# Performance work log

Measured on AMD Instinct MI355X. Metric: run time of the kernel, lower is better.

The kernel has to match this reference:

```python
import jax, jax.numpy as jnp
import numpy as np

B, C, H, W = 8, 3, 1024, 1024
N_SPOTS = int(H * W * 0.015)  # 15728, matches torch: n = int(H*W*0.015)
KSIZE, SIGMA = 5, 1.5
RMAX = 3  # max snow-box radius (torch.randint(1, 4))


def setup_inputs() -> dict:
    key = jax.random.key(0)
    k1, k2, k3, k4 = jax.random.split(key, 4)
    x = jax.random.uniform(k1, (B, C, H, W), dtype=jnp.float32)
    ys = jax.random.randint(k2, (B, N_SPOTS), 0, H)
    xs = jax.random.randint(k3, (B, N_SPOTS), 0, W)
    rs = jax.random.randint(k4, (B, N_SPOTS), 0, 3)  # radius = rs + 1 in {1,2,3}
    return {"x": x, "ys": ys, "xs": xs, "rs": rs}


def _snow_mask(ys, xs, rs, h, w):
    # Union of axis-aligned boxes: pixel (py,px) is snow iff some spot has
    # |py - y| <= r and |px - x| <= r (box clipping to the image is equivalent).
    b, n = ys.shape
    r = rs + 1  # radii 1..3
    d = jnp.arange(-RMAX, RMAX + 1)
    dy = jnp.repeat(d, 2 * RMAX + 1)  # [49]
    dx = jnp.tile(d, 2 * RMAX + 1)    # [49]
    yy = ys[:, :, None] + dy  # [B, n, 49]
    xx = xs[:, :, None] + dx
    valid = ((jnp.abs(dy) <= r[:, :, None]) & (jnp.abs(dx) <= r[:, :, None])
             & (yy >= 0) & (yy < h) & (xx >= 0) & (xx < w))
    yy = jnp.where(valid, yy, h)  # out-of-bounds sentinel -> dropped by scatter
    xx = jnp.where(valid, xx, w)
    b_idx = jnp.broadcast_to(jnp.arange(b)[:, None, None], yy.shape)
    mask = jnp.zeros((b, h, w), dtype=bool)
    mask = mask.at[b_idx, yy, xx].set(True, mode="drop")
    return mask


def _gauss_kernel():
    coords = jnp.arange(KSIZE, dtype=jnp.float32) - KSIZE // 2
    g = jnp.exp(-coords ** 2 / (2.0 * SIGMA ** 2))
    g = g / g.sum()
    return jnp.outer(g, g)  # [5, 5]


def reference(x, ys, xs, rs):
    b, c, h, w = x.shape
    mask = _snow_mask(ys, xs, rs, h, w)                   # [B, H, W]
    out = jnp.where(mask[:, None, :, :], jnp.float32(0.95), x)
    kernel = jnp.broadcast_to(_gauss_kernel(), (c, 1, KSIZE, KSIZE))  # depthwise OIHW
    pad = KSIZE // 2
    out = jax.lax.conv_general_dilated(
        out, kernel, window_strides=(1, 1), padding=[(pad, pad), (pad, pad)],
        dimension_numbers=("NCHW", "OIHW", "NCHW"), feature_group_count=c)
    return jnp.clip(out, 0.0, 1.0)
```

## Files before the change

kernel.cpp:

```cpp
#include <hip/hip_runtime.h>

#define BB 8
#define CC 3
#define HH 1024
#define WW 1024
#define NS 15728

#define G0 0.1200784f
#define G1 0.2338808f
#define G2 0.2920816f

__global__ __launch_bounds__(256) void snow_mask_kernel(
    const int* __restrict__ ys, const int* __restrict__ xs,
    const int* __restrict__ rs, unsigned int* __restrict__ mbits) {
  int s = blockIdx.x * 256 + threadIdx.x;
  if (s >= NS) return;
  int b = blockIdx.y;
  int idx = b * NS + s;
  int y = ys[idx];
  int x = xs[idx];
  int r = rs[idx] + 1;
  int x0 = max(x - r, 0), x1 = min(x + r, WW - 1);
  int y0 = max(y - r, 0), y1 = min(y + r, HH - 1);
  int w0 = x0 >> 5, w1 = x1 >> 5;
  unsigned int m0 = 0xFFFFFFFFu << (x0 & 31);
  unsigned int m1 = 0xFFFFFFFFu >> (31 - (x1 & 31));
  for (int py = y0; py <= y1; ++py) {
    unsigned int* rowp = mbits + ((unsigned)(b * HH + py) << 5);
    if (w0 == w1) {
      atomicOr(&rowp[w0], m0 & m1);
    } else {
      atomicOr(&rowp[w0], m0);
      atomicOr(&rowp[w1], m1);
    }
  }
}

#define TS 140
#define NLOAD 2312

__global__ __launch_bounds__(256, 4) void snow_blur_kernel(
    const float* __restrict__ x, const unsigned int* __restrict__ mbits,
    float* __restrict__ out) {
  __shared__ float tile[68 * TS];

  const int bz = blockIdx.z;
  const int b = bz / CC;
  const int bx = blockIdx.x, by = blockIdx.y;
  const int tid = threadIdx.x;
  const float* __restrict__ xp = x + (size_t)bz * (HH * WW);
  const unsigned int* __restrict__ mb = mbits + ((unsigned)(b * HH) << 5);

  const int gxbase = bx * 128 - 4;
  const int gybase = by * 64 - 2;

  float4 v[10];
  unsigned int bits[10];
  int lidx[10];
#pragma unroll
  for (int k = 0; k < 10; ++k) {
    int i = tid + k * 256;
    i = i < (NLOAD - 1) ? i : (NLOAD - 1);
    int r = i / 34;
    int c4 = i - r * 34;
    int gy = gybase + r;
    int gx = gxbase + c4 * 4;
    int gyc = min(max(gy, 0), HH - 1);
    int gxc = min(max(gx, 0), WW - 4);
    v[k] = *(const float4*)(xp + (size_t)gyc * WW + gxc);
    unsigned int bm = (mb[(gyc << 5) + (gxc >> 5)] >> (gxc & 31)) & 0xFu;
    if ((gy != gyc) | (gx != gxc)) bm = 16u;
    bits[k] = bm;
    lidx[k] = r * TS + c4 * 4;
  }
#pragma unroll
  for (int k = 0; k < 10; ++k) {
    float4 t = v[k];
    unsigned int bm = bits[k];
    if (bm & 1u) t.x = 0.95f;
    if (bm & 2u) t.y = 0.95f;
    if (bm & 4u) t.z = 0.95f;
    if (bm & 8u) t.w = 0.95f;
    if (bm & 16u) { t.x = 0.f; t.y = 0.f; t.z = 0.f; t.w = 0.f; }
    *(float4*)&tile[lidx[k]] = t;
  }
  __syncthreads();

  const int c = tid & 31;
  const int ty = tid >> 5;
  const float* trow = tile + (ty * 8) * TS + c * 4;

  auto hrow = [&](int j, float4& h) {
    const float* p = trow + j * TS;
    float4 A = *(const float4*)(p);
    float4 Bv = *(const float4*)(p + 4);
    float2 Cv = *(const float2*)(p + 8);
    h.x = G0 * (A.z + Bv.z) + G1 * (A.w + Bv.y) + G2 * Bv.x;
    h.y = G0 * (A.w + Bv.w) + G1 * (Bv.x + Bv.z) + G2 * Bv.y;
    h.z = G0 * (Bv.x + Cv.x) + G1 * (Bv.y + Bv.w) + G2 * Bv.z;
    h.w = G0 * (Bv.y + Cv.y) + G1 * (Bv.z + Cv.x) + G2 * Bv.w;
  };

  float4 h0, h1, h2, h3, h4;
  hrow(0, h0); hrow(1, h1); hrow(2, h2); hrow(3, h3); hrow(4, h4);

  float* op = out + (size_t)bz * (HH * WW) +
              (size_t)(by * 64 + ty * 8) * WW + (bx * 128 + c * 4);
#pragma unroll
  for (int k = 0; k < 8; ++k) {
    float4 s;
    s.x = G0 * (h0.x + h4.x) + G1 * (h1.x + h3.x) + G2 * h2.x;
    s.y = G0 * (h0.y + h4.y) + G1 * (h1.y + h3.y) + G2 * h2.y;
    s.z = G0 * (h0.z + h4.z) + G1 * (h1.z + h3.z) + G2 * h2.z;
    s.w = G0 * (h0.w + h4.w) + G1 * (h1.w + h3.w) + G2 * h2.w;
    s.x = fminf(fmaxf(s.x, 0.f), 1.f);
    s.y = fminf(fmaxf(s.y, 0.f), 1.f);
    s.z = fminf(fmaxf(s.z, 0.f), 1.f);
    s.w = fminf(fmaxf(s.w, 0.f), 1.f);
    *(float4*)op = s;
    op += WW;
    h0 = h1; h1 = h2; h2 = h3; h3 = h4;
    if (k < 7) hrow(k + 5, h4);
  }
}

extern "C" void kernel_launch(void* const* d_in, const int* in_sizes, int n_in,
                              void* d_out, int out_size, void* d_ws, size_t ws_size,
                              hipStream_t stream) {
  const float* x = (const float*)d_in[0];
  const int* ys = (const int*)d_in[1];
  const int* xs = (const int*)d_in[2];
  const int* rs = (const int*)d_in[3];
  float* out = (float*)d_out;

  unsigned int* mbits = (unsigned int*)d_ws;
  hipMemsetAsync(mbits, 0, (size_t)BB * HH * WW / 8, stream);

  dim3 mgrid((NS + 255) / 256, BB);
  snow_mask_kernel<<<mgrid, 256, 0, stream>>>(ys, xs, rs, mbits);

  dim3 grid(WW / 128, HH / 64, BB * CC);
  snow_blur_kernel<<<grid, 256, 0, stream>>>(x, mbits, out);
}
```

Before: 212.0 us.

## Build snow mask per column stripe in LDS and blur from registers without shared tile

```diff
diff --git a/kernel.cpp b/kernel.cpp
--- a/kernel.cpp
+++ b/kernel.cpp
@@ -10,104 +10,131 @@
 #define G1 0.2338808f
 #define G2 0.2920816f
 
+#define NSTRIPE 16
+#define STRW 64
+
 __global__ __launch_bounds__(256) void snow_mask_kernel(
     const int* __restrict__ ys, const int* __restrict__ xs,
     const int* __restrict__ rs, unsigned int* __restrict__ mbits) {
-  int s = blockIdx.x * 256 + threadIdx.x;
-  if (s >= NS) return;
-  int b = blockIdx.y;
-  int idx = b * NS + s;
-  int y = ys[idx];
-  int x = xs[idx];
-  int r = rs[idx] + 1;
-  int x0 = max(x - r, 0), x1 = min(x + r, WW - 1);
-  int y0 = max(y - r, 0), y1 = min(y + r, HH - 1);
-  int w0 = x0 >> 5, w1 = x1 >> 5;
-  unsigned int m0 = 0xFFFFFFFFu << (x0 & 31);
-  unsigned int m1 = 0xFFFFFFFFu >> (31 - (x1 & 31));
-  for (int py = y0; py <= y1; ++py) {
-    unsigned int* rowp = mbits + ((unsigned)(b * HH + py) << 5);
+  __shared__ unsigned int lm[HH * 2];
+  const int b = blockIdx.y;
+  const int sx0 = blockIdx.x * STRW;
+  const int tid = threadIdx.x;
+
+  for (int i = tid; i < HH * 2; i += 256) lm[i] = 0u;
+  __syncthreads();
+
+  for (int s = tid; s < NS; s += 256) {
+    int idx = b * NS + s;
+    int y = ys[idx];
+    int x = xs[idx];
+    int r = rs[idx] + 1;
+    int x0 = max(x - r, sx0), x1 = min(x + r, sx0 + (STRW - 1));
+    if (x0 > x1) continue;
+    int y0 = max(y - r, 0), y1 = min(y + r, HH - 1);
+    int lx0 = x0 - sx0, lx1 = x1 - sx0;
+    int w0 = lx0 >> 5, w1 = lx1 >> 5;
+    unsigned m0 = 0xFFFFFFFFu << (lx0 & 31);
+    unsigned m1 = 0xFFFFFFFFu >> (31 - (lx1 & 31));
     if (w0 == w1) {
-      atomicOr(&rowp[w0], m0 & m1);
+      unsigned m = m0 & m1;
+      for (int py = y0; py <= y1; ++py) atomicOr(&lm[(py << 1) + w0], m);
     } else {
-      atomicOr(&rowp[w0], m0);
-      atomicOr(&rowp[w1], m1);
+      for (int py = y0; py <= y1; ++py) {
+        atomicOr(&lm[(py << 1) + 0], m0);
+        atomicOr(&lm[(py << 1) + 1], m1);
+      }
     }
+  }
+  __syncthreads();
+
+  unsigned int* dst = mbits + (((unsigned)(b * HH)) << 5) + blockIdx.x * 2;
+  for (int i = tid; i < HH * 2; i += 256) {
+    dst[((i >> 1) << 5) + (i & 1)] = lm[i];
   }
 }
 
-#define TS 140
-#define NLOAD 2312
+#define RROWS 16
 
-__global__ __launch_bounds__(256, 4) void snow_blur_kernel(
+__global__ __launch_bounds__(256, 6) void snow_blur_kernel(
     const float* __restrict__ x, const unsigned int* __restrict__ mbits,
     float* __restrict__ out) {
-  __shared__ float tile[68 * TS];
+  const int bz = blockIdx.y;
+  const int b = bz / CC;
+  const int gy0 = blockIdx.x * RROWS;
+  const int tid = threadIdx.x;
+  const int col = tid << 2;
 
-  const int bz = blockIdx.z;
-  const int b = bz / CC;
-  const int bx = blockIdx.x, by = blockIdx.y;
-  const int tid = threadIdx.x;
   const float* __restrict__ xp = x + (size_t)bz * (HH * WW);
-  const unsigned int* __restrict__ mb = mbits + ((unsigned)(b * HH) << 5);
+  const unsigned int* __restrict__ mb = mbits + (((unsigned)(b * HH)) << 5);
 
-  const int gxbase = bx * 128 - 4;
-  const int gybase = by * 64 - 2;
+  const int colLc = max(col - 4, 0);
+  const int colRc = min(col + 4, WW - 4);
+  const unsigned loob16 = (col == 0) ? 16u : 0u;
+  const unsigned roob16 = (col == WW - 4) ? 16u : 0u;
+  const int mwL = colLc >> 5, shL = colLc & 31;
+  const int s5 = col & 31;
+  const int mwR = colRc >> 5, shR = colRc & 31;
 
-  float4 v[10];
-  unsigned int bits[10];
-  int lidx[10];
-#pragma unroll
-  for (int k = 0; k < 10; ++k) {
-    int i = tid + k * 256;
-    i = i < (NLOAD - 1) ? i : (NLOAD - 1);
-    int r = i / 34;
-    int c4 = i - r * 34;
-    int gy = gybase + r;
-    int gx = gxbase + c4 * 4;
+  auto loadrow = [&](int gy, float4& A, float4& Bv, float4& Cv,
+                     unsigned& wl, unsigned& wr, unsigned& ro) {
     int gyc = min(max(gy, 0), HH - 1);
-    int gxc = min(max(gx, 0), WW - 4);
-    v[k] = *(const float4*)(xp + (size_t)gyc * WW + gxc);
-    unsigned int bm = (mb[(gyc << 5) + (gxc >> 5)] >> (gxc & 31)) & 0xFu;
-    if ((gy != gyc) | (gx != gxc)) bm = 16u;
-    bits[k] = bm;
-    lidx[k] = r * TS + c4 * 4;
-  }
-#pragma unroll
-  for (int k = 0; k < 10; ++k) {
-    float4 t = v[k];
-    unsigned int bm = bits[k];
-    if (bm & 1u) t.x = 0.95f;
-    if (bm & 2u) t.y = 0.95f;
-    if (bm & 4u) t.z = 0.95f;
-    if (bm & 8u) t.w = 0.95f;
-    if (bm & 16u) { t.x = 0.f; t.y = 0.f; t.z = 0.f; t.w = 0.f; }
-    *(float4*)&tile[lidx[k]] = t;
-  }
-  __syncthreads();
+    ro = (gy != gyc) ? 16u : 0u;
+    const float* rp = xp + ((size_t)gyc << 10);
+    const unsigned* mrow = mb + (gyc << 5);
+    A = *(const float4*)(rp + colLc);
+    Bv = *(const float4*)(rp + col);
+    Cv = *(const float4*)(rp + colRc);
+    wl = mrow[mwL];
+    wr = mrow[mwR];
+  };
 
-  const int c = tid & 31;
-  const int ty = tid >> 5;
-  const float* trow = tile + (ty * 8) * TS + c * 4;
+  auto fix4 = [](float4 v, unsigned m) {
+    float4 t;
+    t.x = (m & 1u) ? 0.95f : v.x;
+    t.y = (m & 2u) ? 0.95f : v.y;
+    t.z = (m & 4u) ? 0.95f : v.z;
+    t.w = (m & 8u) ? 0.95f : v.w;
+    if (m & 16u) { t.x = 0.f; t.y = 0.f; t.z = 0.f; t.w = 0.f; }
+    return t;
+  };
 
-  auto hrow = [&](int j, float4& h) {
-    const float* p = trow + j * TS;
-    float4 A = *(const float4*)(p);
-    float4 Bv = *(const float4*)(p + 4);
-    float2 Cv = *(const float2*)(p + 8);
-    h.x = G0 * (A.z + Bv.z) + G1 * (A.w + Bv.y) + G2 * Bv.x;
-    h.y = G0 * (A.w + Bv.w) + G1 * (Bv.x + Bv.z) + G2 * Bv.y;
-    h.z = G0 * (Bv.x + Cv.x) + G1 * (Bv.y + Bv.w) + G2 * Bv.z;
-    h.w = G0 * (Bv.y + Cv.y) + G1 * (Bv.z + Cv.x) + G2 * Bv.w;
+  auto hrow = [&](float4 A, float4 Bv, float4 Cv,
+                  unsigned wl, unsigned wr, unsigned ro) {
+    unsigned wc = (s5 == 0) ? wr : wl;
+    unsigned ma = ((wl >> shL) & 0xFu) | ro | loob16;
+    unsigned mbm = ((wc >> s5) & 0xFu) | ro;
+    unsigned mc = ((wr >> shR) & 0xFu) | ro | roob16;
+    float4 fA = fix4(A, ma);
+    float4 fB = fix4(Bv, mbm);
+    float4 fC = fix4(Cv, mc);
+    float4 h;
+    h.x = G0 * (fA.z + fB.z) + G1 * (fA.w + fB.y) + G2 * fB.x;
+    h.y = G0 * (fA.w + fB.w) + G1 * (fB.x + fB.z) + G2 * fB.y;
+    h.z = G0 * (fB.x + fC.x) + G1 * (fB.y + fB.w) + G2 * fB.z;
+    h.w = G0 * (fB.y + fC.y) + G1 * (fB.z + fC.x) + G2 * fB.w;
+    return h;
   };
 
   float4 h0, h1, h2, h3, h4;
-  hrow(0, h0); hrow(1, h1); hrow(2, h2); hrow(3, h3); hrow(4, h4);
+  {
+    float4 A, Bv, Cv; unsigned wl, wr, ro;
+    loadrow(gy0 - 2, A, Bv, Cv, wl, wr, ro); h0 = hrow(A, Bv, Cv, wl, wr, ro);
+    loadrow(gy0 - 1, A, Bv, Cv, wl, wr, ro); h1 = hrow(A, Bv, Cv, wl, wr, ro);
+    loadrow(gy0 + 0, A, Bv, Cv, wl, wr, ro); h2 = hrow(A, Bv, Cv, wl, wr, ro);
+    loadrow(gy0 + 1, A, Bv, Cv, wl, wr, ro); h3 = hrow(A, Bv, Cv, wl, wr, ro);
+  }
+  float4 cA, cB, cC; unsigned cwl, cwr, cro;
+  loadrow(gy0 + 2, cA, cB, cC, cwl, cwr, cro);
 
-  float* op = out + (size_t)bz * (HH * WW) +
-              (size_t)(by * 64 + ty * 8) * WW + (bx * 128 + c * 4);
+  float* op = out + (size_t)bz * (HH * WW) + ((size_t)gy0 << 10) + col;
 #pragma unroll
-  for (int k = 0; k < 8; ++k) {
+  for (int k = 0; k < RROWS; ++k) {
+    float4 nA, nB, nC; unsigned nwl, nwr, nro;
+    loadrow(gy0 + k + 3, nA, nB, nC, nwl, nwr, nro);
+
+    h4 = hrow(cA, cB, cC, cwl, cwr, cro);
+
     float4 s;
     s.x = G0 * (h0.x + h4.x) + G1 * (h1.x + h3.x) + G2 * h2.x;
     s.y = G0 * (h0.y + h4.y) + G1 * (h1.y + h3.y) + G2 * h2.y;
@@ -119,8 +146,9 @@
     s.w = fminf(fmaxf(s.w, 0.f), 1.f);
     *(float4*)op = s;
     op += WW;
+
     h0 = h1; h1 = h2; h2 = h3; h3 = h4;
-    if (k < 7) hrow(k + 5, h4);
+    cA = nA; cB = nB; cC = nC; cwl = nwl; cwr = nwr; cro = nro;
   }
 }
 
@@ -134,11 +162,10 @@
   float* out = (float*)d_out;
 
   unsigned int* mbits = (unsigned int*)d_ws;
-  hipMemsetAsync(mbits, 0, (size_t)BB * HH * WW / 8, stream);
 
-  dim3 mgrid((NS + 255) / 256, BB);
+  dim3 mgrid(NSTRIPE, BB);
   snow_mask_kernel<<<mgrid, 256, 0, stream>>>(ys, xs, rs, mbits);
 
-  dim3 grid(WW / 128, HH / 64, BB * CC);
+  dim3 grid(HH / RROWS, BB * CC);
   snow_blur_kernel<<<grid, 256, 0, stream>>>(x, mbits, out);
 }
```

Measured after the change: 252.5 us. 19.1% more time.
